# Kernel tuning notes

Hardware: AMD Instinct MI355X
Metric: run time of the kernel (lower is better)

## Reference

```python
import jax, jax.numpy as jnp
import numpy as np

N_NODES = 100000
N_EDGES = 1600000
IN_DIM = 64
HID_DIM = 64
NUM_CLASSES = 10
NUM_GRAPHS = 64


def setup_inputs() -> dict:
    key = jax.random.key(0)
    ks = jax.random.split(key, 8)
    x = jax.random.normal(ks[0], (N_NODES, IN_DIM), dtype=jnp.float32)
    edge_index = jax.random.randint(ks[1], (2, N_EDGES), 0, N_NODES, dtype=jnp.int32)
    batch = jnp.sort(jax.random.randint(ks[2], (N_NODES,), 0, NUM_GRAPHS, dtype=jnp.int32))
    # GCNConv weights (glorot-ish scale) and biases
    W1 = jax.random.normal(ks[3], (IN_DIM, HID_DIM), dtype=jnp.float32) / np.sqrt(IN_DIM)
    b1 = jnp.zeros((HID_DIM,), dtype=jnp.float32)
    W2 = jax.random.normal(ks[4], (HID_DIM, HID_DIM), dtype=jnp.float32) / np.sqrt(HID_DIM)
    b2 = jnp.zeros((HID_DIM,), dtype=jnp.float32)
    Wlin = jax.random.normal(ks[5], (HID_DIM, NUM_CLASSES), dtype=jnp.float32) / np.sqrt(HID_DIM)
    blin = jnp.zeros((NUM_CLASSES,), dtype=jnp.float32)
    return {"x": x, "edge_index": edge_index, "batch": batch,
            "W1": W1, "b1": b1, "W2": W2, "b2": b2, "Wlin": Wlin, "blin": blin}


def _gcn_conv(h, src, dst, norm, W, b, n_nodes):
    # h' = scatter_add( norm * (h W)[src] -> dst ) + b   (symmetric-normalized A+I)
    m = (h @ W)[src] * norm[:, None]          # [E+N, hid] edge messages (incl. self-loops)
    out = jax.ops.segment_sum(m, dst, num_segments=n_nodes)
    return out + b


def reference(x, edge_index, batch, W1, b1, W2, b2, Wlin, blin):
    n = x.shape[0]
    loops = jnp.arange(n, dtype=edge_index.dtype)
    src = jnp.concatenate([edge_index[0], loops])  # A + I self-loops
    dst = jnp.concatenate([edge_index[1], loops])
    deg = jax.ops.segment_sum(jnp.ones_like(dst, dtype=x.dtype), dst, num_segments=n)
    dinv = jax.lax.rsqrt(jnp.maximum(deg, 1.0))
    norm = dinv[src] * dinv[dst]               # D^{-1/2} (A+I) D^{-1/2} edge weights

    h = jax.nn.relu(_gcn_conv(x, src, dst, norm, W1, b1, n))
    h = jax.nn.relu(_gcn_conv(h, src, dst, norm, W2, b2, n))

    # global_mean_pool over batch segments
    sums = jax.ops.segment_sum(h, batch, num_segments=NUM_GRAPHS)
    cnts = jax.ops.segment_sum(jnp.ones((n,), dtype=h.dtype), batch, num_segments=NUM_GRAPHS)
    pooled = sums / jnp.maximum(cnts, 1.0)[:, None]
    return pooled @ Wlin + blin                # [G, num_classes]
```

## Files before the change

kernel.cpp:

```cpp
#include <hip/hip_runtime.h>
#include <hip/hip_bf16.h>


#define NDIM 64
#define NGRAPH 64
#define NREP 32
#define BSHIFT 7
#define BNODES 128
#define ECHUNK 8192

__device__ __forceinline__ unsigned short f32_to_bf16(float f) {
    unsigned int u = __float_as_uint(f);
    unsigned int r = 0x7FFFu + ((u >> 16) & 1u);
    return (unsigned short)((u + r) >> 16);
}

__global__ void bincnt_k(const int* __restrict__ dst, int* __restrict__ cntmat,
                         int e, int nb) {
    extern __shared__ int hist[];
    int t = threadIdx.x;
    for (int i = t; i < nb; i += 256) hist[i] = 0;
    __syncthreads();
    int base = blockIdx.x * ECHUNK + t;
#pragma unroll
    for (int k = 0; k < 32; ++k) {
        int i = base + k * 256;
        if (i < e) atomicAdd(&hist[dst[i] >> BSHIFT], 1);
    }
    __syncthreads();
    long row = (long)blockIdx.x * nb;
    for (int i = t; i < nb; i += 256) cntmat[row + i] = hist[i];
}

__global__ void colscan_k(const int* __restrict__ cntmat, int* __restrict__ basemat,
                          int* __restrict__ bucketTot, int nblk, int nb) {
    __shared__ int s[256];
    int b = blockIdx.x;
    int t = threadIdx.x;
    int v = (t < nblk) ? cntmat[(long)t * nb + b] : 0;
    s[t] = v;
    __syncthreads();
    for (int off = 1; off < 256; off <<= 1) {
        int tmp = (t >= off) ? s[t - off] : 0;
        __syncthreads();
        s[t] += tmp;
        __syncthreads();
    }
    if (t < nblk) basemat[(long)t * nb + b] = s[t] - v;
    if (t == 255) bucketTot[b] = s[255];
}

__global__ void bscan_k(const int* __restrict__ bucketTot, int* __restrict__ bucketStart,
                        int* __restrict__ start, int nb, int n, int e) {
    __shared__ int s[1024];
    int t = threadIdx.x;
    int v = (t < nb) ? bucketTot[t] : 0;
    s[t] = v;
    __syncthreads();
    for (int off = 1; off < 1024; off <<= 1) {
        int tmp = (t >= off) ? s[t - off] : 0;
        __syncthreads();
        s[t] += tmp;
        __syncthreads();
    }
    if (t < nb) bucketStart[t + 1] = s[t];
    if (t == 0) { bucketStart[0] = 0; start[n] = e; }
}

__global__ void bscatter_k(const int* __restrict__ src, const int* __restrict__ dst,
                           const int* __restrict__ bucketStart,
                           const int* __restrict__ basemat,
                           unsigned int* __restrict__ ebuf, int e, int nb) {
    extern __shared__ int cur[];
    int t = threadIdx.x;
    long row = (long)blockIdx.x * nb;
    for (int i = t; i < nb; i += 256) cur[i] = bucketStart[i] + basemat[row + i];
    __syncthreads();
    int base = blockIdx.x * ECHUNK + t;
#pragma unroll
    for (int k = 0; k < 32; ++k) {
        int i = base + k * 256;
        if (i < e) {
            int d = dst[i];
            int b = d >> BSHIFT;
            int pos = atomicAdd(&cur[b], 1);
            ebuf[pos] = ((unsigned)(d & (BNODES - 1)) << 25) | (unsigned)src[i];
        }
    }
}

__global__ void fill2_k(const unsigned int* __restrict__ ebuf,
                        const int* __restrict__ bucketStart,
                        const int* __restrict__ batch, float* __restrict__ dinv,
                        int* __restrict__ start, int* __restrict__ csr,
                        int* __restrict__ gstart, int* __restrict__ gend, int n) {
    __shared__ int scnt[BNODES], sincl[BNODES], scur[BNODES];
    int t = threadIdx.x;
    int b = blockIdx.x;
    int node0 = b << BSHIFT;
    int nNodes = min(BNODES, n - node0);
    if (t < BNODES) scnt[t] = 0;
    int e0 = bucketStart[b], e1 = bucketStart[b + 1];
    __syncthreads();
    for (int i = e0 + t; i < e1; i += 256)
        atomicAdd(&scnt[ebuf[i] >> 25], 1);
    __syncthreads();
    int val = (t < BNODES) ? scnt[t] : 0;
    if (t < BNODES) sincl[t] = val;
    __syncthreads();
    for (int off = 1; off < BNODES; off <<= 1) {
        int tmp = (t >= off && t < BNODES) ? sincl[t - off] : 0;
        __syncthreads();
        if (t < BNODES) sincl[t] += tmp;
        __syncthreads();
    }
    if (t < nNodes) {
        int v = node0 + t;
        int st = e0 + sincl[t] - val;
        start[v] = st;
        scur[t] = st;
        dinv[v] = rsqrtf((float)(val + 1));
        int g = batch[v];
        if (v == 0 || batch[v - 1] != g) gstart[g] = v;
        if (v == n - 1 || batch[v + 1] != g) gend[g] = v + 1;
    }
    __syncthreads();
    for (int i = e0 + t; i < e1; i += 256) {
        unsigned rec = ebuf[i];
        int pos = atomicAdd(&scur[rec >> 25], 1);
        csr[pos] = (int)(rec & 0x1FFFFFFu);
    }
}

__global__ void gemm_k(const float* __restrict__ A, const float* __restrict__ W,
                       const float* __restrict__ scale,
                       unsigned long long* __restrict__ C, int n) {
    __shared__ float4 Wl4[64 * 16];
    __shared__ float4 Xl4[64 * 16];
    int t = threadIdx.x;
    const float4* W4 = (const float4*)W;
#pragma unroll
    for (int i = 0; i < 4; ++i) Wl4[t + 256 * i] = W4[t + 256 * i];
    const float4* A4 = (const float4*)A;
    long fbase = (long)blockIdx.x * 1024;
    long fmax  = (long)n * 16;
#pragma unroll
    for (int i = 0; i < 4; ++i) {
        long f = fbase + t + 256 * i;
        float4 v;
        if (f < fmax) v = A4[f];
        else { v.x = 0.f; v.y = 0.f; v.z = 0.f; v.w = 0.f; }
        Xl4[t + 256 * i] = v;
    }
    __syncthreads();
    int rg = t >> 4, cg = t & 15;
    float a00 = 0.f, a01 = 0.f, a02 = 0.f, a03 = 0.f;
    float a10 = 0.f, a11 = 0.f, a12 = 0.f, a13 = 0.f;
    float a20 = 0.f, a21 = 0.f, a22 = 0.f, a23 = 0.f;
    float a30 = 0.f, a31 = 0.f, a32 = 0.f, a33 = 0.f;
#pragma unroll 4
    for (int k4 = 0; k4 < 16; ++k4) {
        float4 w0 = Wl4[(4 * k4 + 0) * 16 + cg];
        float4 w1 = Wl4[(4 * k4 + 1) * 16 + cg];
        float4 w2 = Wl4[(4 * k4 + 2) * 16 + cg];
        float4 w3 = Wl4[(4 * k4 + 3) * 16 + cg];
        float4 x0 = Xl4[(4 * rg + 0) * 16 + k4];
        float4 x1 = Xl4[(4 * rg + 1) * 16 + k4];
        float4 x2 = Xl4[(4 * rg + 2) * 16 + k4];
        float4 x3 = Xl4[(4 * rg + 3) * 16 + k4];
        a00 += x0.x * w0.x + x0.y * w1.x + x0.z * w2.x + x0.w * w3.x;
        a01 += x0.x * w0.y + x0.y * w1.y + x0.z * w2.y + x0.w * w3.y;
        a02 += x0.x * w0.z + x0.y * w1.z + x0.z * w2.z + x0.w * w3.z;
        a03 += x0.x * w0.w + x0.y * w1.w + x0.z * w2.w + x0.w * w3.w;
        a10 += x1.x * w0.x + x1.y * w1.x + x1.z * w2.x + x1.w * w3.x;
        a11 += x1.x * w0.y + x1.y * w1.y + x1.z * w2.y + x1.w * w3.y;
        a12 += x1.x * w0.z + x1.y * w1.z + x1.z * w2.z + x1.w * w3.z;
        a13 += x1.x * w0.w + x1.y * w1.w + x1.z * w2.w + x1.w * w3.w;
        a20 += x2.x * w0.x + x2.y * w1.x + x2.z * w2.x + x2.w * w3.x;
        a21 += x2.x * w0.y + x2.y * w1.y + x2.z * w2.y + x2.w * w3.y;
        a22 += x2.x * w0.z + x2.y * w1.z + x2.z * w2.z + x2.w * w3.z;
        a23 += x2.x * w0.w + x2.y * w1.w + x2.z * w2.w + x2.w * w3.w;
        a30 += x3.x * w0.x + x3.y * w1.x + x3.z * w2.x + x3.w * w3.x;
        a31 += x3.x * w0.y + x3.y * w1.y + x3.z * w2.y + x3.w * w3.y;
        a32 += x3.x * w0.z + x3.y * w1.z + x3.z * w2.z + x3.w * w3.z;
        a33 += x3.x * w0.w + x3.y * w1.w + x3.z * w2.w + x3.w * w3.w;
    }
    int vb = blockIdx.x * 64 + rg * 4;
    int v;
    float s;
    unsigned long long u;
    v = vb + 0;
    if (v < n) {
        s = scale[v];
        u  = (unsigned long long)(((unsigned int)f32_to_bf16(s * a01) << 16) | (unsigned int)f32_to_bf16(s * a00));
        u |= (unsigned long long)(((unsigned int)f32_to_bf16(s * a03) << 16) | (unsigned int)f32_to_bf16(s * a02)) << 32;
        C[(long)v * 16 + cg] = u;
    }
    v = vb + 1;
    if (v < n) {
        s = scale[v];
        u  = (unsigned long long)(((unsigned int)f32_to_bf16(s * a11) << 16) | (unsigned int)f32_to_bf16(s * a10));
        u |= (unsigned long long)(((unsigned int)f32_to_bf16(s * a13) << 16) | (unsigned int)f32_to_bf16(s * a12)) << 32;
        C[(long)v * 16 + cg] = u;
    }
    v = vb + 2;
    if (v < n) {
        s = scale[v];
        u  = (unsigned long long)(((unsigned int)f32_to_bf16(s * a21) << 16) | (unsigned int)f32_to_bf16(s * a20));
        u |= (unsigned long long)(((unsigned int)f32_to_bf16(s * a23) << 16) | (unsigned int)f32_to_bf16(s * a22)) << 32;
        C[(long)v * 16 + cg] = u;
    }
    v = vb + 3;
    if (v < n) {
        s = scale[v];
        u  = (unsigned long long)(((unsigned int)f32_to_bf16(s * a31) << 16) | (unsigned int)f32_to_bf16(s * a30));
        u |= (unsigned long long)(((unsigned int)f32_to_bf16(s * a33) << 16) | (unsigned int)f32_to_bf16(s * a32)) << 32;
        C[(long)v * 16 + cg] = u;
    }
}

__device__ __forceinline__ float gather_row(const unsigned int* __restrict__ xp,
                                            const int* __restrict__ csr,
                                            int s0, int d0, int h, int p, int v) {
    float l0 = 0.f, l1 = 0.f, l2 = 0.f, l3 = 0.f;
    float h0 = 0.f, h1 = 0.f, h2 = 0.f, h3 = 0.f;
    int i = 0;
    for (; i + 16 <= d0; i += 16) {
        int j0 = csr[s0 + i +  0 + h];
        int j1 = csr[s0 + i +  2 + h];
        int j2 = csr[s0 + i +  4 + h];
        int j3 = csr[s0 + i +  6 + h];
        int j4 = csr[s0 + i +  8 + h];
        int j5 = csr[s0 + i + 10 + h];
        int j6 = csr[s0 + i + 12 + h];
        int j7 = csr[s0 + i + 14 + h];
        unsigned int u0 = xp[(long)j0 * 32 + p];
        unsigned int u1 = xp[(long)j1 * 32 + p];
        unsigned int u2 = xp[(long)j2 * 32 + p];
        unsigned int u3 = xp[(long)j3 * 32 + p];
        unsigned int u4 = xp[(long)j4 * 32 + p];
        unsigned int u5 = xp[(long)j5 * 32 + p];
        unsigned int u6 = xp[(long)j6 * 32 + p];
        unsigned int u7 = xp[(long)j7 * 32 + p];
        l0 += __uint_as_float(u0 << 16);  h0 += __uint_as_float(u0 & 0xFFFF0000u);
        l1 += __uint_as_float(u1 << 16);  h1 += __uint_as_float(u1 & 0xFFFF0000u);
        l2 += __uint_as_float(u2 << 16);  h2 += __uint_as_float(u2 & 0xFFFF0000u);
        l3 += __uint_as_float(u3 << 16);  h3 += __uint_as_float(u3 & 0xFFFF0000u);
        l0 += __uint_as_float(u4 << 16);  h0 += __uint_as_float(u4 & 0xFFFF0000u);
        l1 += __uint_as_float(u5 << 16);  h1 += __uint_as_float(u5 & 0xFFFF0000u);
        l2 += __uint_as_float(u6 << 16);  h2 += __uint_as_float(u6 & 0xFFFF0000u);
        l3 += __uint_as_float(u7 << 16);  h3 += __uint_as_float(u7 & 0xFFFF0000u);
    }
    for (; i + 8 <= d0; i += 8) {
        int j0 = csr[s0 + i + 0 + h];
        int j1 = csr[s0 + i + 2 + h];
        int j2 = csr[s0 + i + 4 + h];
        int j3 = csr[s0 + i + 6 + h];
        unsigned int u0 = xp[(long)j0 * 32 + p];
        unsigned int u1 = xp[(long)j1 * 32 + p];
        unsigned int u2 = xp[(long)j2 * 32 + p];
        unsigned int u3 = xp[(long)j3 * 32 + p];
        l0 += __uint_as_float(u0 << 16);  h0 += __uint_as_float(u0 & 0xFFFF0000u);
        l1 += __uint_as_float(u1 << 16);  h1 += __uint_as_float(u1 & 0xFFFF0000u);
        l2 += __uint_as_float(u2 << 16);  h2 += __uint_as_float(u2 & 0xFFFF0000u);
        l3 += __uint_as_float(u3 << 16);  h3 += __uint_as_float(u3 & 0xFFFF0000u);
    }
    for (; i + 4 <= d0; i += 4) {
        int j0 = csr[s0 + i + 0 + h];
        int j1 = csr[s0 + i + 2 + h];
        unsigned int u0 = xp[(long)j0 * 32 + p];
        unsigned int u1 = xp[(long)j1 * 32 + p];
        l0 += __uint_as_float(u0 << 16);  h0 += __uint_as_float(u0 & 0xFFFF0000u);
        l1 += __uint_as_float(u1 << 16);  h1 += __uint_as_float(u1 & 0xFFFF0000u);
    }
    for (; i + 2 <= d0; i += 2) {
        int j = csr[s0 + i + h];
        unsigned int u = xp[(long)j * 32 + p];
        l0 += __uint_as_float(u << 16);
        h0 += __uint_as_float(u & 0xFFFF0000u);
    }
    if (i < d0 && h == 0) {
        int j = csr[s0 + i];
        unsigned int u = xp[(long)j * 32 + p];
        l0 += __uint_as_float(u << 16);
        h0 += __uint_as_float(u & 0xFFFF0000u);
    }
    float al = (l0 + l1) + (l2 + l3);
    float ah = (h0 + h1) + (h2 + h3);
    al += __shfl_xor(al, 32);
    ah += __shfl_xor(ah, 32);
    unsigned int us = xp[(long)v * 32 + p];
    al += __uint_as_float(us << 16);
    ah += __uint_as_float(us & 0xFFFF0000u);
    return h ? ah : al;
}

__global__ void agg_k(const unsigned int* __restrict__ xp, const float* __restrict__ dinv,
                      const int* __restrict__ start, const int* __restrict__ csr,
                      const float* __restrict__ bias, float* __restrict__ out, int n) {
    int t = threadIdx.x;
    int lane = t & 63;
    int h = lane >> 5;
    int p = lane & 31;
    int v = blockIdx.x * 4 + (t >> 6);
    if (v >= n) return;
    int s0 = start[v];
    int d0 = start[v + 1] - s0;
    float sum = gather_row(xp, csr, s0, d0, h, p, v);
    int d = 2 * p + h;
    float val = sum * dinv[v] + bias[d];
    out[(long)v * NDIM + d] = fmaxf(val, 0.f);
}

__global__ void aggpool_k(const unsigned int* __restrict__ xp, const float* __restrict__ dinv,
                          const int* __restrict__ start, const int* __restrict__ csr,
                          const float* __restrict__ b2, const int* __restrict__ batch,
                          float* __restrict__ pooledR, int n) {
    int t = threadIdx.x;
    int lane = t & 63;
    int h = lane >> 5, p = lane & 31;
    int wid = blockIdx.x * 4 + (t >> 6);
    int v0 = wid * 4;
    if (v0 >= n) return;
    int v1 = min(v0 + 4, n);
    int d = 2 * p + h;
    float bias = b2[d];
    long rbase = (long)(wid & (NREP - 1)) * (NGRAPH * NDIM);
    int gcur = -1;
    float acc = 0.f;
    for (int v = v0; v < v1; ++v) {
        int g = batch[v];
        if (g != gcur) {
            if (gcur >= 0) atomicAdd(&pooledR[rbase + gcur * NDIM + d], acc);
            gcur = g;
            acc = 0.f;
        }
        int s0 = start[v];
        int d0 = start[v + 1] - s0;
        float sum = gather_row(xp, csr, s0, d0, h, p, v);
        acc += fmaxf(sum * dinv[v] + bias, 0.f);
    }
    if (gcur >= 0) atomicAdd(&pooledR[rbase + gcur * NDIM + d], acc);
}

__global__ void reduce_k(const float* __restrict__ pooledR, float* __restrict__ pooled) {
    int t = blockIdx.x * 256 + threadIdx.x;
    if (t >= NGRAPH * NDIM) return;
    float s = 0.f;
    for (int r = 0; r < NREP; ++r) s += pooledR[(long)r * (NGRAPH * NDIM) + t];
    pooled[t] = s;
}

__global__ void final_k(const float* __restrict__ pooled, const int* __restrict__ gstart,
                        const int* __restrict__ gend,
                        const float* __restrict__ Wlin, const float* __restrict__ blin,
                        float* __restrict__ out, int nclass) {
    int t = blockIdx.x * blockDim.x + threadIdx.x;
    if (t >= NGRAPH * nclass) return;
    int g = t / nclass, c = t % nclass;
    float cnt = (float)(gend[g] - gstart[g]);
    float inv = 1.f / fmaxf(cnt, 1.f);
    float acc = 0.f;
    for (int j = 0; j < NDIM; ++j) acc += pooled[g * NDIM + j] * Wlin[j * nclass + c];
    out[t] = acc * inv + blin[c];
}

extern "C" void kernel_launch(void* const* d_in, const int* in_sizes, int n_in,
                              void* d_out, int out_size, void* d_ws, size_t ws_size,
                              hipStream_t stream) {
    const float* x     = (const float*)d_in[0];
    const int*   ei    = (const int*)d_in[1];
    const int*   batch = (const int*)d_in[2];
    const float* W1    = (const float*)d_in[3];
    const float* b1    = (const float*)d_in[4];
    const float* W2    = (const float*)d_in[5];
    const float* b2    = (const float*)d_in[6];
    const float* Wlin  = (const float*)d_in[7];
    const float* blin  = (const float*)d_in[8];
    float* out = (float*)d_out;

    const int N = in_sizes[0] / NDIM;
    const int E = in_sizes[1] / 2;
    const int NCLASS = in_sizes[7] / NDIM;
    const int* src = ei;
    const int* dst = ei + E;
    const int NB   = (N + BNODES - 1) >> BSHIFT;
    const int NBLK = (E + ECHUNK - 1) / ECHUNK;

    size_t o = 0;
    char* wsp = (char*)d_ws;
    auto take = [&](size_t nbytes) -> void* {
        void* p = (void*)(wsp + o);
        o += (nbytes + 255) & ~(size_t)255;
        return p;
    };
    int*   gstart    = (int*)take(NGRAPH * 4);
    int*   gend      = (int*)take(NGRAPH * 4);
    float* pooledR   = (float*)take((size_t)NREP * NGRAPH * NDIM * 4);
    size_t zero_bytes = o;
    float* pooled    = (float*)take(NGRAPH * NDIM * 4);
    int*   cntmat   = (int*)take((size_t)NBLK * NB * 4);
    int*   basemat  = (int*)take((size_t)NBLK * NB * 4);
    int*   bucketTot   = (int*)take((size_t)NB * 4);
    int*   bucketStart = (int*)take((size_t)(NB + 1) * 4);
    float* dinv  = (float*)take((size_t)N * 4);
    int*   start = (int*)take((size_t)(N + 1) * 4);
    int*   csr   = (int*)take((size_t)E * 4);
    unsigned int* ebuf = (unsigned int*)take((size_t)E * 4);
    unsigned int* xws  = (unsigned int*)take((size_t)N * NDIM * 2);
    float* h     = (float*)take((size_t)N * NDIM * 4);
    (void)ws_size;

    hipMemsetAsync(d_ws, 0, zero_bytes, stream);

    int rbl = (N + 3) / 4;
    int gbl = (N + 63) / 64;
    int pbl = (N + 15) / 16;

    bincnt_k<<<NBLK, 256, (size_t)NB * 4, stream>>>(dst, cntmat, E, NB);
    colscan_k<<<NB, 256, 0, stream>>>(cntmat, basemat, bucketTot, NBLK, NB);
    bscan_k<<<1, 1024, 0, stream>>>(bucketTot, bucketStart, start, NB, N, E);
    bscatter_k<<<NBLK, 256, (size_t)NB * 4, stream>>>(src, dst, bucketStart, basemat, ebuf, E, NB);
    fill2_k<<<NB, 256, 0, stream>>>(ebuf, bucketStart, batch, dinv, start, csr, gstart, gend, N);

    gemm_k<<<gbl, 256, 0, stream>>>(x, W1, dinv, (unsigned long long*)xws, N);
    agg_k<<<rbl, 256, 0, stream>>>(xws, dinv, start, csr, b1, h, N);
    gemm_k<<<gbl, 256, 0, stream>>>(h, W2, dinv, (unsigned long long*)xws, N);
    aggpool_k<<<pbl, 256, 0, stream>>>(xws, dinv, start, csr, b2, batch, pooledR, N);
    reduce_k<<<(NGRAPH * NDIM + 255) / 256, 256, 0, stream>>>(pooledR, pooled);
    final_k<<<(NGRAPH * NCLASS + 255) / 256, 256, 0, stream>>>(pooled, gstart, gend, Wlin, blin, out, NCLASS);
}
```

Baseline: 276.8 us.

## Store layer-1 activations as bf16, shrink edge chunks, fold pool reduction into final

The first aggregation now writes its ReLU output as packed bf16 instead of fp32. A new GEMM kernel reads that bf16 input, which halves the traffic for the intermediate hidden tensor. The edge-bucketing chunk size drops from 8192 to 2048 so the histogram and scatter launches have more blocks, and the column scan grows to 1024 threads to cover the larger block count. The separate reduce kernel is removed and its replica summation moves into final_k, saving one launch. The cost is extra rounding of the intermediate activations and more redundant pooledR reads inside final_k.

```diff
diff --git a/kernel.cpp b/kernel.cpp
--- a/kernel.cpp
+++ b/kernel.cpp
@@ -7,7 +7,7 @@
 #define NREP 32
 #define BSHIFT 7
 #define BNODES 128
-#define ECHUNK 8192
+#define ECHUNK 2048
 
 __device__ __forceinline__ unsigned short f32_to_bf16(float f) {
     unsigned int u = __float_as_uint(f);
@@ -23,7 +23,7 @@
     __syncthreads();
     int base = blockIdx.x * ECHUNK + t;
 #pragma unroll
-    for (int k = 0; k < 32; ++k) {
+    for (int k = 0; k < 8; ++k) {
         int i = base + k * 256;
         if (i < e) atomicAdd(&hist[dst[i] >> BSHIFT], 1);
     }
@@ -34,27 +34,10 @@
 
 __global__ void colscan_k(const int* __restrict__ cntmat, int* __restrict__ basemat,
                           int* __restrict__ bucketTot, int nblk, int nb) {
-    __shared__ int s[256];
+    __shared__ int s[1024];
     int b = blockIdx.x;
     int t = threadIdx.x;
     int v = (t < nblk) ? cntmat[(long)t * nb + b] : 0;
-    s[t] = v;
-    __syncthreads();
-    for (int off = 1; off < 256; off <<= 1) {
-        int tmp = (t >= off) ? s[t - off] : 0;
-        __syncthreads();
-        s[t] += tmp;
-        __syncthreads();
-    }
-    if (t < nblk) basemat[(long)t * nb + b] = s[t] - v;
-    if (t == 255) bucketTot[b] = s[255];
-}
-
-__global__ void bscan_k(const int* __restrict__ bucketTot, int* __restrict__ bucketStart,
-                        int* __restrict__ start, int nb, int n, int e) {
-    __shared__ int s[1024];
-    int t = threadIdx.x;
-    int v = (t < nb) ? bucketTot[t] : 0;
     s[t] = v;
     __syncthreads();
     for (int off = 1; off < 1024; off <<= 1) {
@@ -63,6 +46,23 @@
         s[t] += tmp;
         __syncthreads();
     }
+    if (t < nblk) basemat[(long)t * nb + b] = s[t] - v;
+    if (t == 1023) bucketTot[b] = s[1023];
+}
+
+__global__ void bscan_k(const int* __restrict__ bucketTot, int* __restrict__ bucketStart,
+                        int* __restrict__ start, int nb, int n, int e) {
+    __shared__ int s[1024];
+    int t = threadIdx.x;
+    int v = (t < nb) ? bucketTot[t] : 0;
+    s[t] = v;
+    __syncthreads();
+    for (int off = 1; off < 1024; off <<= 1) {
+        int tmp = (t >= off) ? s[t - off] : 0;
+        __syncthreads();
+        s[t] += tmp;
+        __syncthreads();
+    }
     if (t < nb) bucketStart[t + 1] = s[t];
     if (t == 0) { bucketStart[0] = 0; start[n] = e; }
 }
@@ -78,7 +78,7 @@
     __syncthreads();
     int base = blockIdx.x * ECHUNK + t;
 #pragma unroll
-    for (int k = 0; k < 32; ++k) {
+    for (int k = 0; k < 8; ++k) {
         int i = base + k * 256;
         if (i < e) {
             int d = dst[i];
@@ -219,6 +219,95 @@
     }
 }
 
+__global__ void gemmb_k(const unsigned long long* __restrict__ A8, const float* __restrict__ W,
+                        const float* __restrict__ scale,
+                        unsigned long long* __restrict__ C, int n) {
+    __shared__ float4 Wl4[64 * 16];
+    __shared__ float4 Xl4[64 * 16];
+    int t = threadIdx.x;
+    const float4* W4 = (const float4*)W;
+#pragma unroll
+    for (int i = 0; i < 4; ++i) Wl4[t + 256 * i] = W4[t + 256 * i];
+    long ubase = (long)blockIdx.x * 1024;
+    long umax  = (long)n * 16;
+#pragma unroll
+    for (int i = 0; i < 4; ++i) {
+        long f = ubase + t + 256 * i;
+        unsigned long long u = (f < umax) ? A8[f] : 0ull;
+        float4 v;
+        v.x = __uint_as_float((unsigned int)(u & 0xFFFFu) << 16);
+        v.y = __uint_as_float((unsigned int)u & 0xFFFF0000u);
+        v.z = __uint_as_float((unsigned int)((u >> 32) & 0xFFFFu) << 16);
+        v.w = __uint_as_float((unsigned int)(u >> 48) << 16);
+        Xl4[t + 256 * i] = v;
+    }
+    __syncthreads();
+    int rg = t >> 4, cg = t & 15;
+    float a00 = 0.f, a01 = 0.f, a02 = 0.f, a03 = 0.f;
+    float a10 = 0.f, a11 = 0.f, a12 = 0.f, a13 = 0.f;
+    float a20 = 0.f, a21 = 0.f, a22 = 0.f, a23 = 0.f;
+    float a30 = 0.f, a31 = 0.f, a32 = 0.f, a33 = 0.f;
+#pragma unroll 4
+    for (int k4 = 0; k4 < 16; ++k4) {
+        float4 w0 = Wl4[(4 * k4 + 0) * 16 + cg];
+        float4 w1 = Wl4[(4 * k4 + 1) * 16 + cg];
+        float4 w2 = Wl4[(4 * k4 + 2) * 16 + cg];
+        float4 w3 = Wl4[(4 * k4 + 3) * 16 + cg];
+        float4 x0 = Xl4[(4 * rg + 0) * 16 + k4];
+        float4 x1 = Xl4[(4 * rg + 1) * 16 + k4];
+        float4 x2 = Xl4[(4 * rg + 2) * 16 + k4];
+        float4 x3 = Xl4[(4 * rg + 3) * 16 + k4];
+        a00 += x0.x * w0.x + x0.y * w1.x + x0.z * w2.x + x0.w * w3.x;
+        a01 += x0.x * w0.y + x0.y * w1.y + x0.z * w2.y + x0.w * w3.y;
+        a02 += x0.x * w0.z + x0.y * w1.z + x0.z * w2.z + x0.w * w3.z;
+        a03 += x0.x * w0.w + x0.y * w1.w + x0.z * w2.w + x0.w * w3.w;
+        a10 += x1.x * w0.x + x1.y * w1.x + x1.z * w2.x + x1.w * w3.x;
+        a11 += x1.x * w0.y + x1.y * w1.y + x1.z * w2.y + x1.w * w3.y;
+        a12 += x1.x * w0.z + x1.y * w1.z + x1.z * w2.z + x1.w * w3.z;
+        a13 += x1.x * w0.w + x1.y * w1.w + x1.z * w2.w + x1.w * w3.w;
+        a20 += x2.x * w0.x + x2.y * w1.x + x2.z * w2.x + x2.w * w3.x;
+        a21 += x2.x * w0.y + x2.y * w1.y + x2.z * w2.y + x2.w * w3.y;
+        a22 += x2.x * w0.z + x2.y * w1.z + x2.z * w2.z + x2.w * w3.z;
+        a23 += x2.x * w0.w + x2.y * w1.w + x2.z * w2.w + x2.w * w3.w;
+        a30 += x3.x * w0.x + x3.y * w1.x + x3.z * w2.x + x3.w * w3.x;
+        a31 += x3.x * w0.y + x3.y * w1.y + x3.z * w2.y + x3.w * w3.y;
+        a32 += x3.x * w0.z + x3.y * w1.z + x3.z * w2.z + x3.w * w3.z;
+        a33 += x3.x * w0.w + x3.y * w1.w + x3.z * w2.w + x3.w * w3.w;
+    }
+    int vb = blockIdx.x * 64 + rg * 4;
+    int v;
+    float s;
+    unsigned long long u;
+    v = vb + 0;
+    if (v < n) {
+        s = scale[v];
+        u  = (unsigned long long)(((unsigned int)f32_to_bf16(s * a01) << 16) | (unsigned int)f32_to_bf16(s * a00));
+        u |= (unsigned long long)(((unsigned int)f32_to_bf16(s * a03) << 16) | (unsigned int)f32_to_bf16(s * a02)) << 32;
+        C[(long)v * 16 + cg] = u;
+    }
+    v = vb + 1;
+    if (v < n) {
+        s = scale[v];
+        u  = (unsigned long long)(((unsigned int)f32_to_bf16(s * a11) << 16) | (unsigned int)f32_to_bf16(s * a10));
+        u |= (unsigned long long)(((unsigned int)f32_to_bf16(s * a13) << 16) | (unsigned int)f32_to_bf16(s * a12)) << 32;
+        C[(long)v * 16 + cg] = u;
+    }
+    v = vb + 2;
+    if (v < n) {
+        s = scale[v];
+        u  = (unsigned long long)(((unsigned int)f32_to_bf16(s * a21) << 16) | (unsigned int)f32_to_bf16(s * a20));
+        u |= (unsigned long long)(((unsigned int)f32_to_bf16(s * a23) << 16) | (unsigned int)f32_to_bf16(s * a22)) << 32;
+        C[(long)v * 16 + cg] = u;
+    }
+    v = vb + 3;
+    if (v < n) {
+        s = scale[v];
+        u  = (unsigned long long)(((unsigned int)f32_to_bf16(s * a31) << 16) | (unsigned int)f32_to_bf16(s * a30));
+        u |= (unsigned long long)(((unsigned int)f32_to_bf16(s * a33) << 16) | (unsigned int)f32_to_bf16(s * a32)) << 32;
+        C[(long)v * 16 + cg] = u;
+    }
+}
+
 __device__ __forceinline__ float gather_row(const unsigned int* __restrict__ xp,
                                             const int* __restrict__ csr,
                                             int s0, int d0, int h, int p, int v) {
@@ -297,7 +386,7 @@
 
 __global__ void agg_k(const unsigned int* __restrict__ xp, const float* __restrict__ dinv,
                       const int* __restrict__ start, const int* __restrict__ csr,
-                      const float* __restrict__ bias, float* __restrict__ out, int n) {
+                      const float* __restrict__ bias, unsigned int* __restrict__ hb, int n) {
     int t = threadIdx.x;
     int lane = t & 63;
     int h = lane >> 5;
@@ -308,8 +397,12 @@
     int d0 = start[v + 1] - s0;
     float sum = gather_row(xp, csr, s0, d0, h, p, v);
     int d = 2 * p + h;
-    float val = sum * dinv[v] + bias[d];
-    out[(long)v * NDIM + d] = fmaxf(val, 0.f);
+    float val = fmaxf(sum * dinv[v] + bias[d], 0.f);
+    float other = __shfl_xor(val, 32);
+    if (h == 0) {
+        unsigned int u = ((unsigned int)f32_to_bf16(other) << 16) | (unsigned int)f32_to_bf16(val);
+        hb[(long)v * 32 + p] = u;
+    }
 }
 
 __global__ void aggpool_k(const unsigned int* __restrict__ xp, const float* __restrict__ dinv,
@@ -343,15 +436,7 @@
     if (gcur >= 0) atomicAdd(&pooledR[rbase + gcur * NDIM + d], acc);
 }
 
-__global__ void reduce_k(const float* __restrict__ pooledR, float* __restrict__ pooled) {
-    int t = blockIdx.x * 256 + threadIdx.x;
-    if (t >= NGRAPH * NDIM) return;
-    float s = 0.f;
-    for (int r = 0; r < NREP; ++r) s += pooledR[(long)r * (NGRAPH * NDIM) + t];
-    pooled[t] = s;
-}
-
-__global__ void final_k(const float* __restrict__ pooled, const int* __restrict__ gstart,
+__global__ void final_k(const float* __restrict__ pooledR, const int* __restrict__ gstart,
                         const int* __restrict__ gend,
                         const float* __restrict__ Wlin, const float* __restrict__ blin,
                         float* __restrict__ out, int nclass) {
@@ -361,7 +446,11 @@
     float cnt = (float)(gend[g] - gstart[g]);
     float inv = 1.f / fmaxf(cnt, 1.f);
     float acc = 0.f;
-    for (int j = 0; j < NDIM; ++j) acc += pooled[g * NDIM + j] * Wlin[j * nclass + c];
+    for (int j = 0; j < NDIM; ++j) {
+        float pj = 0.f;
+        for (int r = 0; r < NREP; ++r) pj += pooledR[(long)r * (NGRAPH * NDIM) + g * NDIM + j];
+        acc += pj * Wlin[j * nclass + c];
+    }
     out[t] = acc * inv + blin[c];
 }
 
@@ -398,7 +487,6 @@
     int*   gend      = (int*)take(NGRAPH * 4);
     float* pooledR   = (float*)take((size_t)NREP * NGRAPH * NDIM * 4);
     size_t zero_bytes = o;
-    float* pooled    = (float*)take(NGRAPH * NDIM * 4);
     int*   cntmat   = (int*)take((size_t)NBLK * NB * 4);
     int*   basemat  = (int*)take((size_t)NBLK * NB * 4);
     int*   bucketTot   = (int*)take((size_t)NB * 4);
@@ -408,7 +496,7 @@
     int*   csr   = (int*)take((size_t)E * 4);
     unsigned int* ebuf = (unsigned int*)take((size_t)E * 4);
     unsigned int* xws  = (unsigned int*)take((size_t)N * NDIM * 2);
-    float* h     = (float*)take((size_t)N * NDIM * 4);
+    unsigned int* hb   = (unsigned int*)take((size_t)N * NDIM * 2);
     (void)ws_size;
 
     hipMemsetAsync(d_ws, 0, zero_bytes, stream);
@@ -418,15 +506,14 @@
     int pbl = (N + 15) / 16;
 
     bincnt_k<<<NBLK, 256, (size_t)NB * 4, stream>>>(dst, cntmat, E, NB);
-    colscan_k<<<NB, 256, 0, stream>>>(cntmat, basemat, bucketTot, NBLK, NB);
+    colscan_k<<<NB, 1024, 0, stream>>>(cntmat, basemat, bucketTot, NBLK, NB);
     bscan_k<<<1, 1024, 0, stream>>>(bucketTot, bucketStart, start, NB, N, E);
     bscatter_k<<<NBLK, 256, (size_t)NB * 4, stream>>>(src, dst, bucketStart, basemat, ebuf, E, NB);
     fill2_k<<<NB, 256, 0, stream>>>(ebuf, bucketStart, batch, dinv, start, csr, gstart, gend, N);
 
     gemm_k<<<gbl, 256, 0, stream>>>(x, W1, dinv, (unsigned long long*)xws, N);
-    agg_k<<<rbl, 256, 0, stream>>>(xws, dinv, start, csr, b1, h, N);
-    gemm_k<<<gbl, 256, 0, stream>>>(h, W2, dinv, (unsigned long long*)xws, N);
+    agg_k<<<rbl, 256, 0, stream>>>(xws, dinv, start, csr, b1, hb, N);
+    gemmb_k<<<gbl, 256, 0, stream>>>((const unsigned long long*)hb, W2, dinv, (unsigned long long*)xws, N);
     aggpool_k<<<pbl, 256, 0, stream>>>(xws, dinv, start, csr, b2, batch, pooledR, N);
-    reduce_k<<<(NGRAPH * NDIM + 255) / 256, 256, 0, stream>>>(pooledR, pooled);
-    final_k<<<(NGRAPH * NCLASS + 255) / 256, 256, 0, stream>>>(pooled, gstart, gend, Wlin, blin, out, NCLASS);
-}
+    final_k<<<(NGRAPH * NCLASS + 255) / 256, 256, 0, stream>>>(pooledR, gstart, gend, Wlin, blin, out, NCLASS);
+}
```

Result: slower. 385.7 us (+39.4%).
